# Optimization experiments

Hardware: AMD Instinct MI355X
Metric: run time of the kernel (lower is better)

The kernel has to match this reference:

```python
import jax, jax.numpy as jnp
import numpy as np

B, S, H, HS, BLK = 4, 4096, 16, 1024, 64
D = HS // H


def setup_inputs() -> dict:
    key = jax.random.key(0)
    ks = jax.random.split(key, 7)
    s = np.float32(1.0 / np.sqrt(HS))
    return {
        "hidden_states": jax.random.normal(ks[0], (B, S, HS), jnp.float32),
        "Wq": jax.random.normal(ks[1], (HS, HS), jnp.float32) * s,
        "bq": jax.random.normal(ks[2], (HS,), jnp.float32) * s,
        "Wk": jax.random.normal(ks[3], (HS, HS), jnp.float32) * s,
        "bk": jax.random.normal(ks[4], (HS,), jnp.float32) * s,
        "Wv": jax.random.normal(ks[5], (HS, HS), jnp.float32) * s,
        "bv": jax.random.normal(ks[6], (HS,), jnp.float32) * s,
    }


def reference(hidden_states, Wq, bq, Wk, bk, Wv, bv):
    b, m, _ = hidden_states.shape
    h, d, wm = H, D, BLK
    wn = wm
    nb = m // wm  # number of blocks
    scale = np.float32(1.0 / np.sqrt(d))

    def heads(x):  # [b, m, hs] -> [b, h, m, d]
        return x.reshape(b, m, h, d).transpose(0, 2, 1, 3)

    q = heads(hidden_states @ Wq.T + bq)
    k = heads(hidden_states @ Wk.T + bk)
    v = heads(hidden_states @ Wv.T + bv)

    qb = q.reshape(b, h, nb, wm, d)
    kb = k.reshape(b, h, nb, wn, d)
    vb = v.reshape(b, h, nb, wn, d)

    def attend(qx, kx, vx):  # qx [b,h,Q,d], kx/vx [b,h,K,d]
        scores = jnp.einsum('bhqd,bhkd->bhqk', qx, kx) * scale
        return jnp.einsum('bhqk,bhkd->bhqd', jax.nn.softmax(scores, axis=-1), vx)

    # first block: full attention over all keys
    first_ctx = attend(qb[:, :, 0], k, v)[:, :, None]

    # second block: keys = blocks [0, 1, 2, -1]
    k2 = jnp.concatenate([kb[:, :, 0], kb[:, :, 1], kb[:, :, 2], kb[:, :, -1]], axis=2)
    v2 = jnp.concatenate([vb[:, :, 0], vb[:, :, 1], vb[:, :, 2], vb[:, :, -1]], axis=2)
    second_ctx = attend(qb[:, :, 1], k2, v2)[:, :, None]

    # middle blocks 2..nb-3: sliding window of 3 key blocks + global first/last
    exp_k = jnp.concatenate([kb[:, :, 1:-3], kb[:, :, 2:-2], kb[:, :, 3:-1]], axis=3)  # [b,h,l,3wn,d]
    exp_v = jnp.concatenate([vb[:, :, 1:-3], vb[:, :, 2:-2], vb[:, :, 3:-1]], axis=3)
    mq = qb[:, :, 2:-2]  # [b,h,l,wm,d]
    inner = jnp.einsum('bhlqd,bhlkd->bhlqk', mq, exp_k) * scale
    first_band = jnp.einsum('bhlqd,bhkd->bhlqk', mq, kb[:, :, 0]) * scale
    last_band = jnp.einsum('bhlqd,bhkd->bhlqk', mq, kb[:, :, -1]) * scale
    band = jnp.concatenate([first_band, inner, last_band], axis=-1)  # [b,h,l,wm,5wn]
    aw = jax.nn.softmax(band, axis=-1)
    mid_ctx = jnp.einsum('bhlqk,bhlkd->bhlqd', aw[..., wn:4 * wn], exp_v)
    mid_ctx = mid_ctx + jnp.einsum('bhlqk,bhkd->bhlqd', aw[..., :wn], vb[:, :, 0])
    mid_ctx = mid_ctx + jnp.einsum('bhlqk,bhkd->bhlqd', aw[..., -wn:], vb[:, :, -1])

    # second-to-last block: keys = blocks [0, -3, -2, -1]
    k3 = jnp.concatenate([kb[:, :, 0], kb[:, :, -3], kb[:, :, -2], kb[:, :, -1]], axis=2)
    v3 = jnp.concatenate([vb[:, :, 0], vb[:, :, -3], vb[:, :, -2], vb[:, :, -1]], axis=2)
    second_last_ctx = attend(qb[:, :, -2], k3, v3)[:, :, None]

    # last block: full attention over all keys
    last_ctx = attend(qb[:, :, -1], k, v)[:, :, None]

    ctx = jnp.concatenate([first_ctx, second_ctx, mid_ctx, second_last_ctx, last_ctx], axis=2)
    return ctx.reshape(b, h, m, d).transpose(0, 2, 1, 3).reshape(b, m, h * d)
```

## Files before the change

### kernel.cpp

```cpp
#include <hip/hip_runtime.h>

typedef unsigned short u16;
using f32x4  = __attribute__((ext_vector_type(4))) float;
using bf16x8 = __attribute__((ext_vector_type(8))) short;

#define SEQ 4096
#define HS  1024
#define NHEAD 16
#define DH  64

__device__ __forceinline__ u16 f2bf(float f) {
  unsigned u = __float_as_uint(f);
  unsigned r = (u + 0x7fffu + ((u >> 16) & 1u)) >> 16;
  return (u16)r;
}

__device__ __forceinline__ void gl_lds16(const void* g, void* l) {
  __builtin_amdgcn_global_load_lds(
      (const __attribute__((address_space(1))) unsigned int*)g,
      (__attribute__((address_space(3))) unsigned int*)l, 16, 0, 0);
}

#define LGKM0 asm volatile("s_waitcnt lgkmcnt(0)" ::: "memory")
#define BARR  __builtin_amdgcn_s_barrier()

__global__ void cvt_kernel(const float* __restrict__ src, u16* __restrict__ dst, int n) {
  int idx = blockIdx.x * blockDim.x + threadIdx.x;
  int stride = gridDim.x * blockDim.x;
  for (int i = idx * 4; i < n; i += stride * 4) {
    float4 v = *reinterpret_cast<const float4*>(src + i);
    u16 o0 = f2bf(v.x), o1 = f2bf(v.y), o2 = f2bf(v.z), o3 = f2bf(v.w);
    unsigned lo = (unsigned)o0 | ((unsigned)o1 << 16);
    unsigned hi = (unsigned)o2 | ((unsigned)o3 << 16);
    uint2 pk; pk.x = lo; pk.y = hi;
    *reinterpret_cast<uint2*>(dst + i) = pk;
  }
}

__global__ void cvt_w_kernel(const float* __restrict__ w0, const float* __restrict__ w1,
                             const float* __restrict__ w2,
                             u16* __restrict__ d0, u16* __restrict__ d1, u16* __restrict__ d2,
                             int n) {
  const float* s; u16* d;
  if (blockIdx.y == 0) { s = w0; d = d0; }
  else if (blockIdx.y == 1) { s = w1; d = d1; }
  else { s = w2; d = d2; }
  int idx = blockIdx.x * blockDim.x + threadIdx.x;
  int stride = gridDim.x * blockDim.x;
  for (int i = idx * 4; i < n; i += stride * 4) {
    float4 v = *reinterpret_cast<const float4*>(s + i);
    u16 o0 = f2bf(v.x), o1 = f2bf(v.y), o2 = f2bf(v.z), o3 = f2bf(v.w);
    unsigned lo = (unsigned)o0 | ((unsigned)o1 << 16);
    unsigned hi = (unsigned)o2 | ((unsigned)o3 << 16);
    uint2 pk; pk.x = lo; pk.y = hi;
    *reinterpret_cast<uint2*>(d + i) = pk;
  }
}

__global__ __launch_bounds__(512) void gemm_qkv8(
    const u16* __restrict__ X,
    const u16* __restrict__ Wq, const u16* __restrict__ Wk, const u16* __restrict__ Wv,
    const float* __restrict__ bq, const float* __restrict__ bk, const float* __restrict__ bv,
    u16* __restrict__ Q, u16* __restrict__ K, u16* __restrict__ V) {
  __shared__ u16 lds[65536];

  const int tid = threadIdx.x;
  const int l = tid & 63;
  const int w = tid >> 6;
  const int wr = w >> 2;
  const int wc = w & 3;
  const int c = l & 15;
  const int g = l >> 4;

  int i = blockIdx.x;
  int k8 = i & 7, j8 = i >> 3;
  int w2 = j8 >> 5, r8 = j8 & 31;
  int np = w2 * 4 + (r8 >> 3);
  int mp = k8 * 8 + (r8 & 7);
  const int m0 = mp * 256;
  const int mat = np >> 2;
  const int n0 = (np & 3) * 256;
  const u16* W = (mat == 0) ? Wq : (mat == 1) ? Wk : Wv;
  const float* bias = (mat == 0) ? bq : (mat == 1) ? bk : bv;
  u16* O = (mat == 0) ? Q : (mat == 1) ? K : V;

  f32x4 acc[2][4][4] = {};

  auto stage = [&](const u16* G, int gbase, int ktile, int kh, int which) {
    u16* region = lds + ((ktile & 1) * 32768 + which * 16384 + kh * 8192);
#pragma unroll
    for (int ii = 0; ii < 2; ++ii) {
      int chunk = w * 2 + ii;
      int srow = chunk * 8 + (l >> 3);
      int slot = (l & 7) ^ (l >> 3);
      int grow = srow + ((slot >> 2) << 7);
      int ke = ktile * 64 + kh * 32 + (slot & 3) * 8;
      gl_lds16(G + (size_t)(gbase + grow) * HS + ke, region + chunk * 512);
    }
  };

  auto readA = [&](int cur, int CH, int KH, bf16x8* aq) {
    const char* base = (const char*)lds + cur * 65536 + KH * 16384;
    int colb = (wr * 64 + g * 16) ^ ((c & 7) << 4);
#pragma unroll
    for (int mf = 0; mf < 4; ++mf)
      aq[mf] = *reinterpret_cast<const bf16x8*>(base + (CH * 64 + mf * 16 + c) * 128 + colb);
  };
  auto readB = [&](int cur, int KH, bf16x8* bq2) {
    const char* base = (const char*)lds + cur * 65536 + 32768 + KH * 16384;
    int colb = ((wc >> 1) * 64 + g * 16) ^ ((c & 7) << 4);
#pragma unroll
    for (int nf = 0; nf < 4; ++nf)
      bq2[nf] = *reinterpret_cast<const bf16x8*>(base + ((wc & 1) * 64 + nf * 16 + c) * 128 + colb);
  };
  auto mma16 = [&](bf16x8* aq, bf16x8* bq2, f32x4 (*accr)[4]) {
    __builtin_amdgcn_s_setprio(1);
#pragma unroll
    for (int mf = 0; mf < 4; ++mf)
#pragma unroll
      for (int nf = 0; nf < 4; ++nf)
        accr[mf][nf] = __builtin_amdgcn_mfma_f32_16x16x32_bf16(aq[mf], bq2[nf], accr[mf][nf], 0, 0, 0);
    __builtin_amdgcn_s_setprio(0);
  };

  stage(X, m0, 0, 0, 0); stage(W, n0, 0, 0, 1);
  stage(X, m0, 0, 1, 0); stage(W, n0, 0, 1, 1);
  stage(X, m0, 1, 0, 0); stage(W, n0, 1, 0, 1);
  asm volatile("s_waitcnt vmcnt(4)" ::: "memory");
  BARR;

  for (int j = 0; j < 16; ++j) {
    const int cur = j & 1;
    bf16x8 aq[4], bq2[4];
    readA(cur, 0, 0, aq); readB(cur, 0, bq2);
    if (j + 1 < 16) stage(X, m0, j + 1, 1, 0);
    BARR; LGKM0; mma16(aq, bq2, acc[0]); BARR;
    readA(cur, 1, 0, aq);
    if (j + 1 < 16) stage(W, n0, j + 1, 1, 1);
    BARR; LGKM0; mma16(aq, bq2, acc[1]); BARR;
    readA(cur, 0, 1, aq); readB(cur, 1, bq2);
    if (j + 2 < 16) stage(X, m0, j + 2, 0, 0);
    BARR; LGKM0; mma16(aq, bq2, acc[0]); BARR;
    readA(cur, 1, 1, aq);
    if (j + 2 < 16) stage(W, n0, j + 2, 0, 1);
    BARR; LGKM0; mma16(aq, bq2, acc[1]);
    if (j < 14)       asm volatile("s_waitcnt vmcnt(4)" ::: "memory");
    else if (j == 14) asm volatile("s_waitcnt vmcnt(0)" ::: "memory");
    BARR;
  }

  __syncthreads();
  {
    u16* cst = lds;
#pragma unroll 1
    for (int p = 0; p < 2; ++p) {
      if (wr == p) {
#pragma unroll
        for (int nf = 0; nf < 4; ++nf) {
          int cc = wc * 64 + nf * 16 + c;
          float bval = bias[n0 + cc];
#pragma unroll
          for (int ch = 0; ch < 2; ++ch)
#pragma unroll
            for (int mf = 0; mf < 4; ++mf)
#pragma unroll
              for (int jj = 0; jj < 4; ++jj) {
                int rl = ch * 64 + mf * 16 + g * 4 + jj;
                cst[rl * 260 + cc] = f2bf(acc[ch][mf][nf][jj] + bval);
              }
        }
      }
      __syncthreads();
#pragma unroll
      for (int i2 = 0; i2 < 8; ++i2) {
        int row = i2 * 16 + (tid >> 5);
        int colu = (tid & 31) * 8;
        bf16x8 vv = *reinterpret_cast<const bf16x8*>(cst + row * 260 + colu);
        *reinterpret_cast<bf16x8*>(O + (size_t)(m0 + p * 128 + row) * HS + n0 + colu) = vv;
      }
      __syncthreads();
    }
  }
}

__global__ void bigbird_attn2(const u16* __restrict__ Q, const u16* __restrict__ K,
                              const u16* __restrict__ V, float* __restrict__ OUT,
                              float* __restrict__ Opart, float* __restrict__ MLpart) {
  __shared__ u16 Qs[64 * 64];
  __shared__ u16 Ks[2][64 * 64];
  __shared__ u16 Vt[64 * 72];
  __shared__ u16 Ps[64 * 72];

  const int tid = threadIdx.x;
  const int lane = tid & 63;
  const int w = tid >> 6;
  const int g = lane >> 4;
  const int c = lane & 15;

  int bid = blockIdx.x;
  int L = (bid & 7) * 752 + (bid >> 3);
  int g_bh = L / 94;
  int r = L - g_bh * 94;
  int b = g_bh & 3, h = g_bh >> 2;

  int qb, nkb, seg4 = 0, p = 0;
  bool heavy;
  if (r < 62) {
    heavy = false;
    qb = r + 1;
    nkb = (qb == 1 || qb == 62) ? 4 : 5;
  } else {
    heavy = true;
    int s = r - 62;
    int q2 = s >> 4, seg = s & 15;
    qb = q2 ? 63 : 0; seg4 = seg * 4; nkb = 4;
    p = ((q2 * 16 + h) * 4 + b) * 16 + seg;
  }

  const size_t base_bh = (size_t)b * SEQ * HS + (size_t)h * DH;

  auto kb_of = [&](int it) -> int {
    if (heavy) return seg4 + it;
    if (qb == 1)  return (it == 3) ? 63 : it;
    if (qb == 62) return (it == 0) ? 0 : 60 + it;
    return (it == 0) ? 0 : ((it == 4) ? 63 : qb - 2 + it);
  };

  {
    const u16* qg = Q + base_bh + (size_t)qb * 64 * HS;
#pragma unroll
    for (int t2 = 0; t2 < 2; ++t2) {
      int sub = w * 2 + t2;
      int rr = sub * 8 + (lane >> 3);
      int c16 = (lane & 7) ^ (rr & 7);
      gl_lds16(qg + (size_t)rr * HS + c16 * 8, Qs + sub * 512);
    }
  }
  int kb0 = kb_of(0);
  {
    const u16* kg = K + base_bh + (size_t)kb0 * 64 * HS;
#pragma unroll
    for (int t2 = 0; t2 < 2; ++t2) {
      int sub = w * 2 + t2;
      int rr = sub * 8 + (lane >> 3);
      int c16 = (lane & 7) ^ (rr & 7);
      gl_lds16(kg + (size_t)rr * HS + c16 * 8, Ks[0] + sub * 512);
    }
  }
  bf16x8 vr0, vr1;
  {
    const u16* vg = V + base_bh + (size_t)kb0 * 64 * HS;
    int krow = tid >> 2, dseg = (tid & 3) * 16;
    vr0 = *reinterpret_cast<const bf16x8*>(vg + (size_t)krow * HS + dseg);
    vr1 = *reinterpret_cast<const bf16x8*>(vg + (size_t)krow * HS + dseg + 8);
  }
  __syncthreads();

  bf16x8 qf[2];
#pragma unroll
  for (int ks = 0; ks < 2; ++ks) {
    int rr = w * 16 + c;
    int c16 = (ks * 4 + g) ^ (rr & 7);
    qf[ks] = *reinterpret_cast<const bf16x8*>(Qs + rr * 64 + c16 * 8);
  }

  float m_run = -1e30f, l_run = 0.f;
  f32x4 o_acc[4] = {};
  const float scale = 0.125f;

  for (int it = 0; it < nkb; ++it) {
    const int cur = it & 1;
    {
      int krow = tid >> 2, dseg = (tid & 3) * 16;
#pragma unroll
      for (int j2 = 0; j2 < 8; ++j2) {
        Vt[(dseg + j2) * 72 + krow]     = (u16)vr0[j2];
        Vt[(dseg + 8 + j2) * 72 + krow] = (u16)vr1[j2];
      }
    }
    if (it + 1 < nkb) {
      int kbn = kb_of(it + 1);
      const u16* kg = K + base_bh + (size_t)kbn * 64 * HS;
#pragma unroll
      for (int t2 = 0; t2 < 2; ++t2) {
        int sub = w * 2 + t2;
        int rr = sub * 8 + (lane >> 3);
        int c16 = (lane & 7) ^ (rr & 7);
        gl_lds16(kg + (size_t)rr * HS + c16 * 8, Ks[cur ^ 1] + sub * 512);
      }
      const u16* vg = V + base_bh + (size_t)kbn * 64 * HS;
      int krow = tid >> 2, dseg = (tid & 3) * 16;
      vr0 = *reinterpret_cast<const bf16x8*>(vg + (size_t)krow * HS + dseg);
      vr1 = *reinterpret_cast<const bf16x8*>(vg + (size_t)krow * HS + dseg + 8);
    }

    f32x4 accs[4] = {};
#pragma unroll
    for (int ks = 0; ks < 2; ++ks) {
#pragma unroll
      for (int mf = 0; mf < 4; ++mf) {
        int rr = mf * 16 + c;
        int c16 = (ks * 4 + g) ^ (rr & 7);
        bf16x8 kf = *reinterpret_cast<const bf16x8*>(Ks[cur] + rr * 64 + c16 * 8);
        accs[mf] = __builtin_amdgcn_mfma_f32_16x16x32_bf16(kf, qf[ks], accs[mf], 0, 0, 0);
      }
    }

    float sv[16];
    float smax = -1e30f;
#pragma unroll
    for (int mf = 0; mf < 4; ++mf)
#pragma unroll
      for (int j = 0; j < 4; ++j) {
        float s = accs[mf][j] * scale;
        sv[mf * 4 + j] = s;
        smax = fmaxf(smax, s);
      }
    smax = fmaxf(smax, __shfl_xor(smax, 16));
    smax = fmaxf(smax, __shfl_xor(smax, 32));
    float m_new = fmaxf(m_run, smax);
    float corr = __expf(m_run - m_new);
    float psum = 0.f;
    u16 pb[16];
#pragma unroll
    for (int i = 0; i < 16; ++i) {
      float pv = __expf(sv[i] - m_new);
      psum += pv;
      pb[i] = f2bf(pv);
    }
    psum += __shfl_xor(psum, 16);
    psum += __shfl_xor(psum, 32);
    l_run = l_run * corr + psum;
    m_run = m_new;

#pragma unroll
    for (int j = 0; j < 4; ++j) {
      float cj = __shfl(corr, g * 4 + j);
#pragma unroll
      for (int df = 0; df < 4; ++df) o_acc[df][j] *= cj;
    }

    {
      int rr = w * 16 + c;
#pragma unroll
      for (int mf = 0; mf < 4; ++mf) {
        unsigned lo = (unsigned)pb[mf * 4 + 0] | ((unsigned)pb[mf * 4 + 1] << 16);
        unsigned hi = (unsigned)pb[mf * 4 + 2] | ((unsigned)pb[mf * 4 + 3] << 16);
        uint2 pk; pk.x = lo; pk.y = hi;
        *reinterpret_cast<uint2*>(Ps + rr * 72 + mf * 16 + g * 4) = pk;
      }
    }

    __syncthreads();

#pragma unroll
    for (int ks = 0; ks < 2; ++ks) {
      bf16x8 pf = *reinterpret_cast<const bf16x8*>(Ps + (w * 16 + c) * 72 + ks * 32 + g * 8);
#pragma unroll
      for (int df = 0; df < 4; ++df) {
        bf16x8 vf = *reinterpret_cast<const bf16x8*>(Vt + (df * 16 + c) * 72 + ks * 32 + g * 8);
        o_acc[df] = __builtin_amdgcn_mfma_f32_16x16x32_bf16(pf, vf, o_acc[df], 0, 0, 0);
      }
    }

    __syncthreads();
  }

  if (!heavy) {
#pragma unroll
    for (int j = 0; j < 4; ++j) {
      float lr = __shfl(l_run, g * 4 + j);
      float inv = 1.f / lr;
      int rr = qb * 64 + w * 16 + g * 4 + j;
      size_t rowbase = ((size_t)b * SEQ + rr) * HS + (size_t)h * DH;
#pragma unroll
      for (int df = 0; df < 4; ++df)
        OUT[rowbase + df * 16 + c] = o_acc[df][j] * inv;
    }
  } else {
#pragma unroll
    for (int j = 0; j < 4; ++j) {
      int row = w * 16 + g * 4 + j;
#pragma unroll
      for (int df = 0; df < 4; ++df)
        Opart[(size_t)p * 4096 + row * 64 + df * 16 + c] = o_acc[df][j];
    }
    if (g == 0) {
      int row = w * 16 + c;
      MLpart[(size_t)p * 128 + row * 2]     = m_run;
      MLpart[(size_t)p * 128 + row * 2 + 1] = l_run;
    }
  }
}

__global__ void bigbird_combine(const float* __restrict__ Opart, const float* __restrict__ MLpart,
                                float* __restrict__ OUT) {
  int bid = blockIdx.x >> 2;
  int quarter = blockIdx.x & 3;
  int b = bid & 3; int t = bid >> 2; int h = t & 15; int q2 = t >> 4;
  int qb = q2 ? 63 : 0;
  int w = threadIdx.x >> 6, lane = threadIdx.x & 63;
  int pbase = ((q2 * 16 + h) * 4 + b) * 16;
#pragma unroll 1
  for (int j2 = 0; j2 < 4; ++j2) {
    int rr = quarter * 4 + j2;
    int row = w * 16 + rr;
    float ms[16], ls[16];
    float M = -1e30f;
#pragma unroll
    for (int s = 0; s < 16; ++s) {
      ms[s] = MLpart[(size_t)(pbase + s) * 128 + row * 2];
      ls[s] = MLpart[(size_t)(pbase + s) * 128 + row * 2 + 1];
      M = fmaxf(M, ms[s]);
    }
    float L = 0.f, acc = 0.f;
#pragma unroll
    for (int s = 0; s < 16; ++s) {
      float e = __expf(ms[s] - M);
      L += ls[s] * e;
      acc += e * Opart[(size_t)(pbase + s) * 4096 + row * 64 + lane];
    }
    int rq = qb * 64 + row;
    OUT[((size_t)b * SEQ + rq) * HS + (size_t)h * DH + lane] = acc / L;
  }
}

extern "C" void kernel_launch(void* const* d_in, const int* in_sizes, int n_in,
                              void* d_out, int out_size, void* d_ws, size_t ws_size,
                              hipStream_t stream) {
  const float* X  = (const float*)d_in[0];
  const float* Wq = (const float*)d_in[1];
  const float* bq = (const float*)d_in[2];
  const float* Wk = (const float*)d_in[3];
  const float* bk = (const float*)d_in[4];
  const float* Wv = (const float*)d_in[5];
  const float* bv = (const float*)d_in[6];
  float* out = (float*)d_out;

  u16* Xb  = (u16*)d_ws;
  u16* Wqb = Xb + 16777216;
  u16* Wkb = Wqb + 1048576;
  u16* Wvb = Wkb + 1048576;
  u16* Qb  = Wvb + 1048576;
  u16* Kb  = Qb + 16777216;
  u16* Vb  = Kb + 16777216;

  float* Opart  = (float*)Xb;
  float* MLpart = (float*)Wqb;

  cvt_kernel<<<2048, 256, 0, stream>>>(X, Xb, 16777216);
  cvt_w_kernel<<<dim3(256, 3), 256, 0, stream>>>(Wq, Wk, Wv, Wqb, Wkb, Wvb, 1048576);
  gemm_qkv8<<<768, 512, 0, stream>>>(Xb, Wqb, Wkb, Wvb, bq, bk, bv, Qb, Kb, Vb);
  bigbird_attn2<<<6016, 256, 0, stream>>>(Qb, Kb, Vb, out, Opart, MLpart);
  bigbird_combine<<<512, 256, 0, stream>>>(Opart, MLpart, out);
}
```

Measured before the change: 236.0 us.

## Switch QKV projection GEMM to 32x32x16 MFMA with restructured fragment loads

Replaces the 16x16x32 bf16 MFMA tiles in the QKV projection GEMM with 32x32x16 MFMA, reorganizing the LDS fragment reads and the accumulator layout to match. The inner loop now has two sub-steps per k-tile instead of four, halving the barriers per tile and issuing X and W staging together. This aims to cut LDS read traffic per FLOP and synchronization overhead. The epilogue is rewritten for the 32x32 output register layout, which risks mapping mistakes.

After: 245.6 us. +4.1%, slower.

```diff
diff --git a/kernel.cpp b/kernel.cpp
--- a/kernel.cpp
+++ b/kernel.cpp
@@ -2,6 +2,7 @@
 
 typedef unsigned short u16;
 using f32x4  = __attribute__((ext_vector_type(4))) float;
+using f32x16 = __attribute__((ext_vector_type(16))) float;
 using bf16x8 = __attribute__((ext_vector_type(8))) short;
 
 #define SEQ 4096
@@ -69,8 +70,8 @@
   const int w = tid >> 6;
   const int wr = w >> 2;
   const int wc = w & 3;
-  const int c = l & 15;
-  const int g = l >> 4;
+  const int r5 = l & 31;
+  const int kh2 = l >> 5;
 
   int i = blockIdx.x;
   int k8 = i & 7, j8 = i >> 3;
@@ -84,7 +85,7 @@
   const float* bias = (mat == 0) ? bq : (mat == 1) ? bk : bv;
   u16* O = (mat == 0) ? Q : (mat == 1) ? K : V;
 
-  f32x4 acc[2][4][4] = {};
+  f32x16 acc32[4][2] = {};
 
   auto stage = [&](const u16* G, int gbase, int ktile, int kh, int which) {
     u16* region = lds + ((ktile & 1) * 32768 + which * 16384 + kh * 8192);
@@ -99,27 +100,39 @@
     }
   };
 
-  auto readA = [&](int cur, int CH, int KH, bf16x8* aq) {
+  auto readA = [&](int cur, int KH, bf16x8 (*aq)[2]) {
     const char* base = (const char*)lds + cur * 65536 + KH * 16384;
-    int colb = (wr * 64 + g * 16) ^ ((c & 7) << 4);
+#pragma unroll
+    for (int mf = 0; mf < 4; ++mf) {
+      int srow = mf * 32 + r5;
+#pragma unroll
+      for (int ph = 0; ph < 2; ++ph) {
+        int slot = ((wr << 2) | (ph << 1) | kh2) ^ (srow & 7);
+        aq[mf][ph] = *reinterpret_cast<const bf16x8*>(base + srow * 128 + slot * 16);
+      }
+    }
+  };
+  auto readB = [&](int cur, int KH, bf16x8 (*bq2)[2]) {
+    const char* base = (const char*)lds + cur * 65536 + 32768 + KH * 16384;
+#pragma unroll
+    for (int nf = 0; nf < 2; ++nf) {
+      int srow = (wc & 1) * 64 + nf * 32 + r5;
+#pragma unroll
+      for (int ph = 0; ph < 2; ++ph) {
+        int slot = (((wc >> 1) << 2) | (ph << 1) | kh2) ^ (srow & 7);
+        bq2[nf][ph] = *reinterpret_cast<const bf16x8*>(base + srow * 128 + slot * 16);
+      }
+    }
+  };
+  auto mma = [&](bf16x8 (*aq)[2], bf16x8 (*bq2)[2]) {
+    __builtin_amdgcn_s_setprio(1);
 #pragma unroll
     for (int mf = 0; mf < 4; ++mf)
-      aq[mf] = *reinterpret_cast<const bf16x8*>(base + (CH * 64 + mf * 16 + c) * 128 + colb);
-  };
-  auto readB = [&](int cur, int KH, bf16x8* bq2) {
-    const char* base = (const char*)lds + cur * 65536 + 32768 + KH * 16384;
-    int colb = ((wc >> 1) * 64 + g * 16) ^ ((c & 7) << 4);
-#pragma unroll
-    for (int nf = 0; nf < 4; ++nf)
-      bq2[nf] = *reinterpret_cast<const bf16x8*>(base + ((wc & 1) * 64 + nf * 16 + c) * 128 + colb);
-  };
-  auto mma16 = [&](bf16x8* aq, bf16x8* bq2, f32x4 (*accr)[4]) {
-    __builtin_amdgcn_s_setprio(1);
-#pragma unroll
-    for (int mf = 0; mf < 4; ++mf)
-#pragma unroll
-      for (int nf = 0; nf < 4; ++nf)
-        accr[mf][nf] = __builtin_amdgcn_mfma_f32_16x16x32_bf16(aq[mf], bq2[nf], accr[mf][nf], 0, 0, 0);
+#pragma unroll
+      for (int nf = 0; nf < 2; ++nf) {
+        acc32[mf][nf] = __builtin_amdgcn_mfma_f32_32x32x16_bf16(aq[mf][0], bq2[nf][0], acc32[mf][nf], 0, 0, 0);
+        acc32[mf][nf] = __builtin_amdgcn_mfma_f32_32x32x16_bf16(aq[mf][1], bq2[nf][1], acc32[mf][nf], 0, 0, 0);
+      }
     __builtin_amdgcn_s_setprio(0);
   };
 
@@ -131,19 +144,13 @@
 
   for (int j = 0; j < 16; ++j) {
     const int cur = j & 1;
-    bf16x8 aq[4], bq2[4];
-    readA(cur, 0, 0, aq); readB(cur, 0, bq2);
-    if (j + 1 < 16) stage(X, m0, j + 1, 1, 0);
-    BARR; LGKM0; mma16(aq, bq2, acc[0]); BARR;
-    readA(cur, 1, 0, aq);
-    if (j + 1 < 16) stage(W, n0, j + 1, 1, 1);
-    BARR; LGKM0; mma16(aq, bq2, acc[1]); BARR;
-    readA(cur, 0, 1, aq); readB(cur, 1, bq2);
-    if (j + 2 < 16) stage(X, m0, j + 2, 0, 0);
-    BARR; LGKM0; mma16(aq, bq2, acc[0]); BARR;
-    readA(cur, 1, 1, aq);
-    if (j + 2 < 16) stage(W, n0, j + 2, 0, 1);
-    BARR; LGKM0; mma16(aq, bq2, acc[1]);
+    bf16x8 aq[4][2], bq2[2][2];
+    readA(cur, 0, aq); readB(cur, 0, bq2);
+    if (j + 1 < 16) { stage(X, m0, j + 1, 1, 0); stage(W, n0, j + 1, 1, 1); }
+    BARR; LGKM0; mma(aq, bq2); BARR;
+    readA(cur, 1, aq); readB(cur, 1, bq2);
+    if (j + 2 < 16) { stage(X, m0, j + 2, 0, 0); stage(W, n0, j + 2, 0, 1); }
+    BARR; LGKM0; mma(aq, bq2);
     if (j < 14)       asm volatile("s_waitcnt vmcnt(4)" ::: "memory");
     else if (j == 14) asm volatile("s_waitcnt vmcnt(0)" ::: "memory");
     BARR;
@@ -153,21 +160,20 @@
   {
     u16* cst = lds;
 #pragma unroll 1
-    for (int p = 0; p < 2; ++p) {
-      if (wr == p) {
-#pragma unroll
-        for (int nf = 0; nf < 4; ++nf) {
-          int cc = wc * 64 + nf * 16 + c;
-          float bval = bias[n0 + cc];
-#pragma unroll
-          for (int ch = 0; ch < 2; ++ch)
-#pragma unroll
-            for (int mf = 0; mf < 4; ++mf)
-#pragma unroll
-              for (int jj = 0; jj < 4; ++jj) {
-                int rl = ch * 64 + mf * 16 + g * 4 + jj;
-                cst[rl * 260 + cc] = f2bf(acc[ch][mf][nf][jj] + bval);
-              }
+    for (int pass = 0; pass < 2; ++pass) {
+      if (wr == pass) {
+#pragma unroll
+        for (int nf = 0; nf < 2; ++nf) {
+          int ccol = wc * 64 + nf * 32 + r5;
+          float bval = bias[n0 + ccol];
+#pragma unroll
+          for (int mf = 0; mf < 4; ++mf) {
+#pragma unroll
+            for (int ri = 0; ri < 16; ++ri) {
+              int rl = mf * 32 + (ri & 3) + ((ri >> 2) * 8) + kh2 * 4;
+              cst[rl * 260 + ccol] = f2bf(acc32[mf][nf][ri] + bval);
+            }
+          }
         }
       }
       __syncthreads();
@@ -176,7 +182,7 @@
         int row = i2 * 16 + (tid >> 5);
         int colu = (tid & 31) * 8;
         bf16x8 vv = *reinterpret_cast<const bf16x8*>(cst + row * 260 + colu);
-        *reinterpret_cast<bf16x8*>(O + (size_t)(m0 + p * 128 + row) * HS + n0 + colu) = vv;
+        *reinterpret_cast<bf16x8*>(O + (size_t)(m0 + pass * 128 + row) * HS + n0 + colu) = vv;
       }
       __syncthreads();
     }
```
